# Kernel optimization log

Hardware: AMD Instinct MI355X
Metric: run time of the kernel (lower is better)

The kernel has to match this reference:

```python
import jax, jax.numpy as jnp
import numpy as np

HEADS = 8
DIM = 64      # dim
DH = 64       # dim_head
DK = 24       # dim_k (== dim_head_k * heads, required by reshape in forward)
DHK = 3       # dim_head_k (also conv groups)


def setup_inputs() -> dict:
    key = jax.random.key(0)
    ks = jax.random.split(key, 10)
    b, h, w = 4, 128, 128
    return {
        "x_in": jax.random.normal(ks[0], (b, h, w, DIM), jnp.float32),
        "illu_fea_trans": jax.random.normal(ks[1], (b, h, w, DIM), jnp.float32),
        "illu_map_trans": jax.random.normal(ks[2], (b, h, w, DK), jnp.float32),
        # Linear weights stored as [in, out] (torch stores [out, in]; math y = x @ W_in_out)
        "Wq": jax.random.normal(ks[3], (DIM, HEADS * DH), jnp.float32) * 0.05,
        "Wk": jax.random.normal(ks[4], (DK, HEADS * DHK), jnp.float32) * 0.05,
        "Wv": jax.random.normal(ks[5], (DIM, HEADS * DH), jnp.float32) * 0.05,
        "rescale": jnp.ones((HEADS, 1, 1), jnp.float32),
        "Wp": jax.random.normal(ks[6], (HEADS * DHK, DK), jnp.float32) * 0.05,
        "bp": jax.random.normal(ks[7], (DK,), jnp.float32) * 0.05,
        # grouped conv weights, OIHW: [out=24, in/groups=8, 3, 3]
        "conv1_w": jax.random.normal(ks[8], (DK, DK // DHK, 3, 3), jnp.float32) * 0.05,
        "conv2_w": jax.random.normal(ks[9], (DK, DK // DHK, 3, 3), jnp.float32) * 0.05,
    }


def _gconv(x_nchw, w_oihw):
    return jax.lax.conv_general_dilated(
        x_nchw, w_oihw, window_strides=(1, 1), padding='SAME',
        feature_group_count=DHK,
        dimension_numbers=('NCHW', 'OIHW', 'NCHW'))


def reference(x_in, illu_fea_trans, illu_map_trans, Wq, Wk, Wv, rescale, Wp, bp, conv1_w, conv2_w):
    b, h, w, c = x_in.shape
    n = h * w
    # projections
    q = (x_in.reshape(b, n, c) @ Wq).reshape(b, n, HEADS, DH)
    k_inp = illu_map_trans.reshape(b, n, DK) @ Wk            # [b, n, heads*dhk]
    v = (illu_fea_trans.reshape(b, n, c) @ Wv).reshape(b, n, HEADS, DH)
    kh = k_inp.reshape(b, n, HEADS, DHK)
    q = q / (DIM ** 0.5)  # note: scaled by sqrt(dim), not sqrt(dim_head)
    # channel-wise cross-attention: attn over channel dims, contracting tokens n
    attn = jnp.einsum('bnhk,bnhd->bhkd', kh, q) * rescale[None]  # [b, heads, dhk, dh]
    attn = jax.nn.softmax(attn, axis=-1)
    out = jnp.einsum('bhkd,bnhd->bnkh', attn, v)             # [b, n, dhk, heads]
    out = out.reshape(b, n, DHK * HEADS) @ Wp + bp           # proj
    out = out.reshape(b, h, w, DK)
    # positional branch: two grouped 3x3 convs with exact GELU on k_inp
    kx = k_inp.reshape(b, h, w, DK).transpose(0, 3, 1, 2)    # NCHW
    y = _gconv(kx, conv1_w)
    y = jax.nn.gelu(y, approximate=False)
    y = _gconv(y, conv2_w)
    return out + y.transpose(0, 2, 3, 1)
```

## Files before the change

### kernel.cpp

```cpp
#include <hip/hip_runtime.h>
#include <math.h>

#define HEADS 8
#define DIM   64
#define DK    24
#define DHK   3
#define BB    4
#define HH    128
#define WW    128
#define NN    (HH*WW)
#define QSCALE 0.125f

__global__ __launch_bounds__(256) void s_reduce(
    const float* __restrict__ imap,
    const float* __restrict__ x,
    float* __restrict__ Sp)
{
    __shared__ float part[4*1536];
    const int tid = threadIdx.x;
    const int blk = blockIdx.x;
    const int b = blk >> 8, chunk = blk & 255;
    const int w = tid >> 6, lane = tid & 63;
    const int cq = lane & 15;
    const int ig = lane >> 4;

    const long tok0 = (long)b * NN + chunk * 64 + w * 16;
    const float* xp = x    + tok0 * 64 + cq * 4;
    const float* mp = imap + tok0 * 24 + ig * 6;

    float acc[6][4];
    #pragma unroll
    for (int r = 0; r < 6; ++r)
        #pragma unroll
        for (int q = 0; q < 4; ++q) acc[r][q] = 0.f;

    #pragma unroll 4
    for (int t = 0; t < 16; ++t) {
        float4 xv = *(const float4*)(xp + t * 64);
        float2 m0 = *(const float2*)(mp + t * 24);
        float2 m1 = *(const float2*)(mp + t * 24 + 2);
        float2 m2 = *(const float2*)(mp + t * 24 + 4);
        float mm[6] = {m0.x, m0.y, m1.x, m1.y, m2.x, m2.y};
        #pragma unroll
        for (int r = 0; r < 6; ++r) {
            acc[r][0] += mm[r] * xv.x;
            acc[r][1] += mm[r] * xv.y;
            acc[r][2] += mm[r] * xv.z;
            acc[r][3] += mm[r] * xv.w;
        }
    }

    float* pp = part + w * 1536;
    #pragma unroll
    for (int r = 0; r < 6; ++r) {
        float4 v = {acc[r][0], acc[r][1], acc[r][2], acc[r][3]};
        *(float4*)(pp + (ig * 6 + r) * 64 + cq * 4) = v;
    }
    __syncthreads();

    for (int e = tid; e < 1536; e += 256)
        atomicAdd(&Sp[b * 1536 + e],
                  part[e] + part[1536 + e] + part[3072 + e] + part[4608 + e]);
}

__global__ __launch_bounds__(192) void attn_fused(
    const float* __restrict__ Sp,
    const float* __restrict__ Wk,
    const float* __restrict__ Wq,
    const float* __restrict__ Wv,
    const float* __restrict__ rescale,
    const float* __restrict__ Wp,
    float* __restrict__ Pt)
{
    __shared__ float Sp_l[1536];
    __shared__ float sS[192];
    __shared__ float sP[192];
    __shared__ float Wv_l[64 * 65];

    const int tid = threadIdx.x, blk = blockIdx.x;
    const int b = blk >> 3, h = blk & 7;
    const int k3 = tid >> 6, lane = tid & 63;

    for (int e = tid; e < 1536; e += 192) Sp_l[e] = Sp[b * 1536 + e];
    for (int e = tid; e < 4096; e += 192) {
        int c = e >> 6, d = e & 63;
        Wv_l[c * 65 + d] = Wv[c * 512 + h * 64 + d];
    }
    __syncthreads();

    {
        const float* wk = Wk + (h * 3 + k3);
        float s = 0.f;
        #pragma unroll
        for (int i = 0; i < 24; ++i) s += wk[i * 24] * Sp_l[i * 64 + lane];
        sS[k3 * 64 + lane] = s;
    }
    __syncthreads();

    {
        const float* wq = Wq + h * 64 + lane;
        const float* sr = sS + k3 * 64;
        float a = 0.f;
        for (int c = 0; c < 64; ++c) a += sr[c] * wq[c * 512];
        a *= QSCALE * rescale[h];
        float mx = a;
        #pragma unroll
        for (int off = 32; off >= 1; off >>= 1)
            mx = fmaxf(mx, __shfl_xor(mx, off, 64));
        float e = expf(a - mx);
        float sum = e;
        #pragma unroll
        for (int off = 32; off >= 1; off >>= 1)
            sum += __shfl_xor(sum, off, 64);
        sP[k3 * 64 + lane] = e / sum;
    }
    __syncthreads();

    {
        const float* pr = sP + k3 * 64;
        const float* wv = Wv_l + lane * 65;
        float m = 0.f;
        #pragma unroll
        for (int d = 0; d < 64; ++d) m += pr[d] * wv[d];
        sS[k3 * 64 + lane] = m;
    }
    __syncthreads();

    for (int q = tid; q < 1536; q += 192) {
        int o = q >> 6, c = q & 63;
        float v = 0.f;
        #pragma unroll
        for (int k = 0; k < 3; ++k)
            v += sS[k * 64 + c] * Wp[(k * 8 + h) * 24 + o];
        atomicAdd(&Pt[b * 1536 + o * 64 + c], v);
    }
}

__global__ __launch_bounds__(192, 2) void conv_fused(
    const float* __restrict__ imap, const float* __restrict__ Wk,
    const float* __restrict__ c1w,  const float* __restrict__ fea,
    const float* __restrict__ c2w,  const float* __restrict__ Pt,
    const float* __restrict__ bp,   float* __restrict__ outp)
{
    __shared__ __align__(16) float kbuf[144 * 28];
    __shared__ __align__(16) float y1l[100 * 28];

    const int tid = threadIdx.x;
    const int blk = blockIdx.x;
    const int b = blk >> 8, ti = (blk >> 4) & 15, tj = blk & 15;
    const int i0 = ti * 8, j0 = tj * 8;
    const int o = tid % 24, jj = tid / 24;
    const int g = o >> 3;

    if (tid < 144) {
        const int pi = tid / 12, pj = tid % 12;
        const int gi = i0 + pi - 2, gj = j0 + pj - 2;
        float kv[24];
        #pragma unroll
        for (int j = 0; j < 24; ++j) kv[j] = 0.f;
        if (gi >= 0 && gi < HH && gj >= 0 && gj < WW) {
            const float4* m4 = (const float4*)(imap + (((long)b * HH + gi) * WW + gj) * 24);
            float m[24];
            #pragma unroll
            for (int i = 0; i < 6; ++i) {
                float4 v = m4[i];
                m[4*i+0]=v.x; m[4*i+1]=v.y; m[4*i+2]=v.z; m[4*i+3]=v.w;
            }
            for (int i = 0; i < 24; ++i) {
                float mi = m[i];
                #pragma unroll
                for (int j = 0; j < 24; ++j) kv[j] += mi * Wk[i * 24 + j];
            }
        }
        #pragma unroll
        for (int j = 0; j < 24; ++j) kbuf[tid * 28 + j] = kv[j];
    }
    __syncthreads();

    {
        float wr[8][9];
        {
            const float4* wp = (const float4*)(c1w + o * 72);
            #pragma unroll
            for (int t = 0; t < 18; ++t) ((float4*)wr)[t] = wp[t];
        }
        for (int task = tid; task < 240; task += 192) {
            const int r = task / 24;
            float wc[3][3][8];
            #pragma unroll
            for (int slot = 0; slot < 2; ++slot)
                #pragma unroll
                for (int di = 0; di < 3; ++di) {
                    const float* p = kbuf + ((r + di) * 12 + slot) * 28 + g * 8;
                    *(float4*)&wc[slot][di][0] = *(const float4*)(p);
                    *(float4*)&wc[slot][di][4] = *(const float4*)(p + 4);
                }
            #pragma unroll
            for (int c = 0; c < 10; ++c) {
                const int s2 = (c + 2) % 3;
                #pragma unroll
                for (int di = 0; di < 3; ++di) {
                    const float* p = kbuf + ((r + di) * 12 + (c + 2)) * 28 + g * 8;
                    *(float4*)&wc[s2][di][0] = *(const float4*)(p);
                    *(float4*)&wc[s2][di][4] = *(const float4*)(p + 4);
                }
                float s = 0.f;
                #pragma unroll
                for (int dj = 0; dj < 3; ++dj) {
                    const int sl = (c + dj) % 3;
                    #pragma unroll
                    for (int di = 0; di < 3; ++di)
                        #pragma unroll
                        for (int ic = 0; ic < 8; ++ic)
                            s += wc[sl][di][ic] * wr[ic][di * 3 + dj];
                }
                const int gi = i0 + r - 1, gj = j0 + c - 1;
                float val = 0.f;
                if (gi >= 0 && gi < HH && gj >= 0 && gj < WW)
                    val = 0.5f * s * (1.f + erff(s * 0.70710678f));
                y1l[(r * 10 + c) * 28 + o] = val;
            }
        }
    }
    __syncthreads();

    float wr[8][9];
    {
        const float4* wp = (const float4*)(c2w + o * 72);
        #pragma unroll
        for (int t = 0; t < 18; ++t) ((float4*)wr)[t] = wp[t];
    }

    float acc[8];
    {
        const float bo = bp[o];
        #pragma unroll
        for (int ii = 0; ii < 8; ++ii) acc[ii] = bo;
        const float* PtRow = Pt + b * 1536 + o * 64;
        const float* feaB = fea + (((long)(b * HH + i0)) * WW + (j0 + jj)) * 64;
        for (int cq = 0; cq < 16; ++cq) {
            float4 p = *(const float4*)(PtRow + cq * 4);
            #pragma unroll
            for (int ii = 0; ii < 8; ++ii) {
                float4 f = *(const float4*)(feaB + (long)ii * WW * 64 + cq * 4);
                acc[ii] += f.x * p.x + f.y * p.y + f.z * p.z + f.w * p.w;
            }
        }
    }

    float win[3][3][8];
    #define LROW(R, SLOT)                                                     \
    {                                                                         \
        const float* rp_ = y1l + ((R) * 10 + jj) * 28 + g * 8;                \
        *(float4*)&win[SLOT][0][0] = *(const float4*)(rp_);                   \
        *(float4*)&win[SLOT][0][4] = *(const float4*)(rp_ + 4);               \
        *(float4*)&win[SLOT][1][0] = *(const float4*)(rp_ + 28);              \
        *(float4*)&win[SLOT][1][4] = *(const float4*)(rp_ + 32);              \
        *(float4*)&win[SLOT][2][0] = *(const float4*)(rp_ + 56);              \
        *(float4*)&win[SLOT][2][4] = *(const float4*)(rp_ + 60);              \
    }

    LROW(0, 0)
    LROW(1, 1)
    #pragma unroll
    for (int ii = 0; ii < 8; ++ii) {
        LROW(ii + 2, (ii + 2) % 3)
        float s = 0.f;
        #pragma unroll
        for (int di = 0; di < 3; ++di) {
            const int slot = (ii + di) % 3;
            #pragma unroll
            for (int dj = 0; dj < 3; ++dj)
                #pragma unroll
                for (int ic = 0; ic < 8; ++ic)
                    s += win[slot][dj][ic] * wr[ic][di * 3 + dj];
        }
        outp[((long)((b * HH + i0 + ii) * WW + j0)) * 24 + tid] = acc[ii] + s;
    }
    #undef LROW
}

extern "C" void kernel_launch(void* const* d_in, const int* in_sizes, int n_in,
                              void* d_out, int out_size, void* d_ws, size_t ws_size,
                              hipStream_t stream) {
    const float* x_in    = (const float*)d_in[0];
    const float* fea     = (const float*)d_in[1];
    const float* imap    = (const float*)d_in[2];
    const float* Wq      = (const float*)d_in[3];
    const float* Wk      = (const float*)d_in[4];
    const float* Wv      = (const float*)d_in[5];
    const float* rescale = (const float*)d_in[6];
    const float* Wp      = (const float*)d_in[7];
    const float* bp      = (const float*)d_in[8];
    const float* c1w     = (const float*)d_in[9];
    const float* c2w     = (const float*)d_in[10];
    float* out = (float*)d_out;

    float* ws = (float*)d_ws;
    float* Sp = ws;
    float* Pt = ws + 6144;

    hipMemsetAsync(ws, 0, 12288 * sizeof(float), stream);
    s_reduce<<<1024, 256, 0, stream>>>(imap, x_in, Sp);
    attn_fused<<<32, 192, 0, stream>>>(Sp, Wk, Wq, Wv, rescale, Wp, Pt);
    conv_fused<<<BB * 256, 192, 0, stream>>>(imap, Wk, c1w, fea, c2w, Pt, bp, out);
}
```

Before: 159.2 us.

## Replace atomic S reduction and memset with per-block partials reduced in attn kernel

```diff
diff --git a/kernel.cpp b/kernel.cpp
--- a/kernel.cpp
+++ b/kernel.cpp
@@ -11,20 +11,21 @@
 #define NN    (HH*WW)
 #define QSCALE 0.125f
 
-__global__ __launch_bounds__(256) void s_reduce(
+__global__ __launch_bounds__(1024) void s_reduce(
     const float* __restrict__ imap,
     const float* __restrict__ x,
-    float* __restrict__ Sp)
+    float* __restrict__ Sp_part,
+    float* __restrict__ Pt)
 {
-    __shared__ float part[4*1536];
+    __shared__ float part[16 * 1540];
     const int tid = threadIdx.x;
     const int blk = blockIdx.x;
-    const int b = blk >> 8, chunk = blk & 255;
+    const int b = blk >> 6, chunk = blk & 63;
     const int w = tid >> 6, lane = tid & 63;
     const int cq = lane & 15;
     const int ig = lane >> 4;
 
-    const long tok0 = (long)b * NN + chunk * 64 + w * 16;
+    const long tok0 = (long)b * NN + chunk * 256 + w * 16;
     const float* xp = x    + tok0 * 64 + cq * 4;
     const float* mp = imap + tok0 * 24 + ig * 6;
 
@@ -50,7 +51,7 @@
         }
     }
 
-    float* pp = part + w * 1536;
+    float* pp = part + w * 1540;
     #pragma unroll
     for (int r = 0; r < 6; ++r) {
         float4 v = {acc[r][0], acc[r][1], acc[r][2], acc[r][3]};
@@ -58,13 +59,18 @@
     }
     __syncthreads();
 
-    for (int e = tid; e < 1536; e += 256)
-        atomicAdd(&Sp[b * 1536 + e],
-                  part[e] + part[1536 + e] + part[3072 + e] + part[4608 + e]);
+    for (int e = tid; e < 1536; e += 1024) {
+        float s = 0.f;
+        #pragma unroll
+        for (int ww = 0; ww < 16; ++ww) s += part[ww * 1540 + e];
+        Sp_part[(long)blk * 1536 + e] = s;
+    }
+    if (blk < 4)
+        for (int e = tid; e < 1536; e += 1024) Pt[blk * 1536 + e] = 0.f;
 }
 
-__global__ __launch_bounds__(192) void attn_fused(
-    const float* __restrict__ Sp,
+__global__ __launch_bounds__(256) void attn_fused(
+    const float* __restrict__ Sp_part,
     const float* __restrict__ Wk,
     const float* __restrict__ Wq,
     const float* __restrict__ Wv,
@@ -79,28 +85,39 @@
 
     const int tid = threadIdx.x, blk = blockIdx.x;
     const int b = blk >> 3, h = blk & 7;
-    const int k3 = tid >> 6, lane = tid & 63;
-
-    for (int e = tid; e < 1536; e += 192) Sp_l[e] = Sp[b * 1536 + e];
-    for (int e = tid; e < 4096; e += 192) {
+    const int w = tid >> 6, lane = tid & 63;
+
+    {
+        float s[6] = {0.f, 0.f, 0.f, 0.f, 0.f, 0.f};
+        const float* p = Sp_part + (long)(b * 64) * 1536 + tid;
+        #pragma unroll 8
+        for (int pb = 0; pb < 64; ++pb)
+            #pragma unroll
+            for (int k = 0; k < 6; ++k)
+                s[k] += p[(long)pb * 1536 + k * 256];
+        #pragma unroll
+        for (int k = 0; k < 6; ++k) Sp_l[tid + k * 256] = s[k];
+    }
+    for (int e = tid; e < 4096; e += 256) {
         int c = e >> 6, d = e & 63;
         Wv_l[c * 65 + d] = Wv[c * 512 + h * 64 + d];
     }
     __syncthreads();
 
-    {
-        const float* wk = Wk + (h * 3 + k3);
+    if (w < 3) {
+        const float* wk = Wk + (h * 3 + w);
         float s = 0.f;
         #pragma unroll
         for (int i = 0; i < 24; ++i) s += wk[i * 24] * Sp_l[i * 64 + lane];
-        sS[k3 * 64 + lane] = s;
-    }
-    __syncthreads();
-
-    {
+        sS[w * 64 + lane] = s;
+    }
+    __syncthreads();
+
+    if (w < 3) {
         const float* wq = Wq + h * 64 + lane;
-        const float* sr = sS + k3 * 64;
+        const float* sr = sS + w * 64;
         float a = 0.f;
+        #pragma unroll 8
         for (int c = 0; c < 64; ++c) a += sr[c] * wq[c * 512];
         a *= QSCALE * rescale[h];
         float mx = a;
@@ -112,21 +129,21 @@
         #pragma unroll
         for (int off = 32; off >= 1; off >>= 1)
             sum += __shfl_xor(sum, off, 64);
-        sP[k3 * 64 + lane] = e / sum;
-    }
-    __syncthreads();
-
-    {
-        const float* pr = sP + k3 * 64;
+        sP[w * 64 + lane] = e / sum;
+    }
+    __syncthreads();
+
+    if (w < 3) {
+        const float* pr = sP + w * 64;
         const float* wv = Wv_l + lane * 65;
         float m = 0.f;
         #pragma unroll
         for (int d = 0; d < 64; ++d) m += pr[d] * wv[d];
-        sS[k3 * 64 + lane] = m;
-    }
-    __syncthreads();
-
-    for (int q = tid; q < 1536; q += 192) {
+        sS[w * 64 + lane] = m;
+    }
+    __syncthreads();
+
+    for (int q = tid; q < 1536; q += 256) {
         int o = q >> 6, c = q & 63;
         float v = 0.f;
         #pragma unroll
@@ -296,12 +313,11 @@
     const float* c2w     = (const float*)d_in[10];
     float* out = (float*)d_out;
 
-    float* ws = (float*)d_ws;
-    float* Sp = ws;
-    float* Pt = ws + 6144;
-
-    hipMemsetAsync(ws, 0, 12288 * sizeof(float), stream);
-    s_reduce<<<1024, 256, 0, stream>>>(imap, x_in, Sp);
-    attn_fused<<<32, 192, 0, stream>>>(Sp, Wk, Wq, Wv, rescale, Wp, Pt);
+    float* ws      = (float*)d_ws;
+    float* Sp_part = ws;
+    float* Pt      = ws + 393216;
+
+    s_reduce<<<256, 1024, 0, stream>>>(imap, x_in, Sp_part, Pt);
+    attn_fused<<<32, 256, 0, stream>>>(Sp_part, Wk, Wq, Wv, rescale, Wp, Pt);
     conv_fused<<<BB * 256, 192, 0, stream>>>(imap, Wk, c1w, fea, c2w, Pt, bp, out);
 }
```

Result: no change. 157.7 us (-1.0%).

## Fuse reduce, attention and conv into one persistent kernel with spin-wait sync

Applied to the files above, without the earlier changes.

```diff
diff --git a/kernel.cpp b/kernel.cpp
--- a/kernel.cpp
+++ b/kernel.cpp
@@ -11,144 +11,158 @@
 #define NN    (HH*WW)
 #define QSCALE 0.125f
 
-__global__ __launch_bounds__(256) void s_reduce(
+__global__ __launch_bounds__(192, 4) void mega(
+    const float* __restrict__ x,
+    const float* __restrict__ fea,
     const float* __restrict__ imap,
-    const float* __restrict__ x,
-    float* __restrict__ Sp)
+    const float* __restrict__ Wq,
+    const float* __restrict__ Wk,
+    const float* __restrict__ Wv,
+    const float* __restrict__ rescale,
+    const float* __restrict__ Wp,
+    const float* __restrict__ bp,
+    const float* __restrict__ c1w,
+    const float* __restrict__ c2w,
+    float* __restrict__ Sp_part,
+    float* __restrict__ Sp2,
+    float* __restrict__ Pt,
+    int* __restrict__ sync_,
+    float* __restrict__ outp)
 {
-    __shared__ float part[4*1536];
+    __shared__ __align__(16) float smem[6832];
+    int* cnt   = sync_;
+    int* done1 = sync_ + 4;
+    int* done2 = sync_ + 8;
+
     const int tid = threadIdx.x;
     const int blk = blockIdx.x;
     const int b = blk >> 8, chunk = blk & 255;
-    const int w = tid >> 6, lane = tid & 63;
-    const int cq = lane & 15;
-    const int ig = lane >> 4;
-
-    const long tok0 = (long)b * NN + chunk * 64 + w * 16;
-    const float* xp = x    + tok0 * 64 + cq * 4;
-    const float* mp = imap + tok0 * 24 + ig * 6;
-
-    float acc[6][4];
-    #pragma unroll
-    for (int r = 0; r < 6; ++r)
-        #pragma unroll
-        for (int q = 0; q < 4; ++q) acc[r][q] = 0.f;
-
-    #pragma unroll 4
-    for (int t = 0; t < 16; ++t) {
-        float4 xv = *(const float4*)(xp + t * 64);
-        float2 m0 = *(const float2*)(mp + t * 24);
-        float2 m1 = *(const float2*)(mp + t * 24 + 2);
-        float2 m2 = *(const float2*)(mp + t * 24 + 4);
-        float mm[6] = {m0.x, m0.y, m1.x, m1.y, m2.x, m2.y};
-        #pragma unroll
-        for (int r = 0; r < 6; ++r) {
-            acc[r][0] += mm[r] * xv.x;
-            acc[r][1] += mm[r] * xv.y;
-            acc[r][2] += mm[r] * xv.z;
-            acc[r][3] += mm[r] * xv.w;
-        }
-    }
-
-    float* pp = part + w * 1536;
-    #pragma unroll
-    for (int r = 0; r < 6; ++r) {
-        float4 v = {acc[r][0], acc[r][1], acc[r][2], acc[r][3]};
-        *(float4*)(pp + (ig * 6 + r) * 64 + cq * 4) = v;
-    }
+    const int ti = chunk >> 4, tj = chunk & 15;
+    const int i0 = ti * 8, j0 = tj * 8;
+
+    {
+        const int i24 = tid % 24, c8 = tid / 24;
+        float av[8];
+        #pragma unroll
+        for (int q = 0; q < 8; ++q) av[q] = 0.f;
+        const long pix0 = ((long)(b * HH + i0)) * WW + j0;
+        for (int r = 0; r < 8; ++r) {
+            const float* xr = x    + (pix0 + r * WW) * 64 + c8 * 8;
+            const float* mr = imap + (pix0 + r * WW) * 24 + i24;
+            #pragma unroll
+            for (int cc = 0; cc < 8; ++cc) {
+                float mv = mr[cc * 24];
+                float4 u = *(const float4*)(xr + cc * 64);
+                float4 v = *(const float4*)(xr + cc * 64 + 4);
+                av[0] += mv * u.x; av[1] += mv * u.y;
+                av[2] += mv * u.z; av[3] += mv * u.w;
+                av[4] += mv * v.x; av[5] += mv * v.y;
+                av[6] += mv * v.z; av[7] += mv * v.w;
+            }
+        }
+        float* sp = Sp_part + ((long)(b * 64 + (chunk >> 2))) * 1536 + i24 * 64 + c8 * 8;
+        #pragma unroll
+        for (int q = 0; q < 8; ++q) atomicAdd(sp + q, av[q]);
+    }
+    __threadfence();
     __syncthreads();
-
-    for (int e = tid; e < 1536; e += 256)
-        atomicAdd(&Sp[b * 1536 + e],
-                  part[e] + part[1536 + e] + part[3072 + e] + part[4608 + e]);
-}
-
-__global__ __launch_bounds__(192) void attn_fused(
-    const float* __restrict__ Sp,
-    const float* __restrict__ Wk,
-    const float* __restrict__ Wq,
-    const float* __restrict__ Wv,
-    const float* __restrict__ rescale,
-    const float* __restrict__ Wp,
-    float* __restrict__ Pt)
-{
-    __shared__ float Sp_l[1536];
-    __shared__ float sS[192];
-    __shared__ float sP[192];
-    __shared__ float Wv_l[64 * 65];
-
-    const int tid = threadIdx.x, blk = blockIdx.x;
-    const int b = blk >> 3, h = blk & 7;
-    const int k3 = tid >> 6, lane = tid & 63;
-
-    for (int e = tid; e < 1536; e += 192) Sp_l[e] = Sp[b * 1536 + e];
-    for (int e = tid; e < 4096; e += 192) {
-        int c = e >> 6, d = e & 63;
-        Wv_l[c * 65 + d] = Wv[c * 512 + h * 64 + d];
-    }
-    __syncthreads();
-
-    {
-        const float* wk = Wk + (h * 3 + k3);
-        float s = 0.f;
-        #pragma unroll
-        for (int i = 0; i < 24; ++i) s += wk[i * 24] * Sp_l[i * 64 + lane];
-        sS[k3 * 64 + lane] = s;
-    }
-    __syncthreads();
-
-    {
-        const float* wq = Wq + h * 64 + lane;
-        const float* sr = sS + k3 * 64;
-        float a = 0.f;
-        for (int c = 0; c < 64; ++c) a += sr[c] * wq[c * 512];
-        a *= QSCALE * rescale[h];
-        float mx = a;
-        #pragma unroll
-        for (int off = 32; off >= 1; off >>= 1)
-            mx = fmaxf(mx, __shfl_xor(mx, off, 64));
-        float e = expf(a - mx);
-        float sum = e;
-        #pragma unroll
-        for (int off = 32; off >= 1; off >>= 1)
-            sum += __shfl_xor(sum, off, 64);
-        sP[k3 * 64 + lane] = e / sum;
-    }
-    __syncthreads();
-
-    {
-        const float* pr = sP + k3 * 64;
-        const float* wv = Wv_l + lane * 65;
-        float m = 0.f;
-        #pragma unroll
-        for (int d = 0; d < 64; ++d) m += pr[d] * wv[d];
-        sS[k3 * 64 + lane] = m;
-    }
-    __syncthreads();
-
-    for (int q = tid; q < 1536; q += 192) {
-        int o = q >> 6, c = q & 63;
-        float v = 0.f;
-        #pragma unroll
-        for (int k = 0; k < 3; ++k)
-            v += sS[k * 64 + c] * Wp[(k * 8 + h) * 24 + o];
-        atomicAdd(&Pt[b * 1536 + o * 64 + c], v);
-    }
-}
-
-__global__ __launch_bounds__(192, 2) void conv_fused(
-    const float* __restrict__ imap, const float* __restrict__ Wk,
-    const float* __restrict__ c1w,  const float* __restrict__ fea,
-    const float* __restrict__ c2w,  const float* __restrict__ Pt,
-    const float* __restrict__ bp,   float* __restrict__ outp)
-{
-    __shared__ __align__(16) float kbuf[144 * 28];
-    __shared__ __align__(16) float y1l[100 * 28];
-
-    const int tid = threadIdx.x;
-    const int blk = blockIdx.x;
-    const int b = blk >> 8, ti = (blk >> 4) & 15, tj = blk & 15;
-    const int i0 = ti * 8, j0 = tj * 8;
+    if (tid == 0) atomicAdd(&cnt[b], 1);
+
+    if (chunk >= 8 && chunk < 16) {
+        if (tid == 0)
+            while (__hip_atomic_load(&cnt[b], __ATOMIC_RELAXED, __HIP_MEMORY_SCOPE_AGENT) < 256)
+                __builtin_amdgcn_s_sleep(4);
+        __syncthreads();
+        __threadfence();
+        const int o8 = chunk - 8;
+        const float* p = Sp_part + ((long)(b * 64 + o8 * 8)) * 1536 + tid * 8;
+        float a2[8];
+        #pragma unroll
+        for (int q = 0; q < 8; ++q) a2[q] = 0.f;
+        #pragma unroll
+        for (int pb = 0; pb < 8; ++pb) {
+            float4 u = *(const float4*)(p + (long)pb * 1536);
+            float4 v = *(const float4*)(p + (long)pb * 1536 + 4);
+            a2[0] += u.x; a2[1] += u.y; a2[2] += u.z; a2[3] += u.w;
+            a2[4] += v.x; a2[5] += v.y; a2[6] += v.z; a2[7] += v.w;
+        }
+        float* s2 = Sp2 + b * 1536 + tid * 8;
+        #pragma unroll
+        for (int q = 0; q < 8; ++q) atomicAdd(s2 + q, a2[q]);
+        __threadfence();
+        __syncthreads();
+        if (tid == 0) atomicAdd(&done1[b], 1);
+    }
+    else if (chunk < 8) {
+        const int h = chunk;
+        if (tid == 0)
+            while (__hip_atomic_load(&done1[b], __ATOMIC_RELAXED, __HIP_MEMORY_SCOPE_AGENT) < 8)
+                __builtin_amdgcn_s_sleep(4);
+        __syncthreads();
+        __threadfence();
+        float* Sp_l = smem;
+        float* sS   = smem + 1536;
+        float* sP   = smem + 1760;
+        float* Wv_l = smem + 1984;
+        for (int e = tid; e < 1536; e += 192) Sp_l[e] = Sp2[b * 1536 + e];
+        for (int e = tid; e < 4096; e += 192) {
+            int c = e >> 6, d = e & 63;
+            Wv_l[c * 65 + d] = Wv[c * 512 + h * 64 + d];
+        }
+        __syncthreads();
+
+        const int w3 = tid >> 6, lane = tid & 63;
+        {
+            const float* wk = Wk + (h * 3 + w3);
+            float s = 0.f;
+            #pragma unroll
+            for (int i = 0; i < 24; ++i) s += wk[i * 24] * Sp_l[i * 64 + lane];
+            sS[w3 * 64 + lane] = s;
+        }
+        __syncthreads();
+        {
+            const float* sr = sS + w3 * 64;
+            float a = 0.f;
+            #pragma unroll 8
+            for (int c = 0; c < 64; ++c) a += sr[c] * Wq[c * 512 + h * 64 + lane];
+            a *= QSCALE * rescale[h];
+            float mx = a;
+            #pragma unroll
+            for (int off = 32; off >= 1; off >>= 1)
+                mx = fmaxf(mx, __shfl_xor(mx, off, 64));
+            float e = expf(a - mx);
+            float sum = e;
+            #pragma unroll
+            for (int off = 32; off >= 1; off >>= 1)
+                sum += __shfl_xor(sum, off, 64);
+            sP[w3 * 64 + lane] = e / sum;
+        }
+        __syncthreads();
+        {
+            const float* pr = sP + w3 * 64;
+            const float* wv = Wv_l + lane * 65;
+            float m = 0.f;
+            #pragma unroll
+            for (int d = 0; d < 64; ++d) m += pr[d] * wv[d];
+            sS[w3 * 64 + lane] = m;
+        }
+        __syncthreads();
+        for (int q = tid; q < 1536; q += 192) {
+            int o = q >> 6, c = q & 63;
+            float v = 0.f;
+            #pragma unroll
+            for (int k = 0; k < 3; ++k)
+                v += sS[k * 64 + c] * Wp[(k * 8 + h) * 24 + o];
+            atomicAdd(&Pt[b * 1536 + o * 64 + c], v);
+        }
+        __threadfence();
+        __syncthreads();
+        if (tid == 0) atomicAdd(&done2[b], 1);
+        __syncthreads();
+    }
+
+    float* kbuf = smem;
+    float* y1l  = smem + 4032;
     const int o = tid % 24, jj = tid / 24;
     const int g = o >> 3;
 
@@ -223,6 +237,12 @@
         }
     }
     __syncthreads();
+
+    if (tid == 0)
+        while (__hip_atomic_load(&done2[b], __ATOMIC_RELAXED, __HIP_MEMORY_SCOPE_AGENT) < 8)
+            __builtin_amdgcn_s_sleep(4);
+    __syncthreads();
+    __threadfence();
 
     float wr[8][9];
     {
@@ -296,12 +316,14 @@
     const float* c2w     = (const float*)d_in[10];
     float* out = (float*)d_out;
 
-    float* ws = (float*)d_ws;
-    float* Sp = ws;
-    float* Pt = ws + 6144;
-
-    hipMemsetAsync(ws, 0, 12288 * sizeof(float), stream);
-    s_reduce<<<1024, 256, 0, stream>>>(imap, x_in, Sp);
-    attn_fused<<<32, 192, 0, stream>>>(Sp, Wk, Wq, Wv, rescale, Wp, Pt);
-    conv_fused<<<BB * 256, 192, 0, stream>>>(imap, Wk, c1w, fea, c2w, Pt, bp, out);
+    float* ws      = (float*)d_ws;
+    float* Sp_part = ws;
+    float* Sp2     = ws + 393216;
+    float* Pt      = ws + 399360;
+    int*   sync_   = (int*)(ws + 405504);
+
+    hipMemsetAsync(ws, 0, 405504 * sizeof(float) + 48, stream);
+    mega<<<BB * 256, 192, 0, stream>>>(x_in, fea, imap, Wq, Wk, Wv, rescale,
+                                       Wp, bp, c1w, c2w,
+                                       Sp_part, Sp2, Pt, sync_, out);
 }
```

Result: slower. 433.6 us (+172.3%).
